# Kernel optimization log

Measured on AMD Instinct MI355X. Metric: run time of the kernel, lower is better.

## Reference

```python
import jax, jax.numpy as jnp
import numpy as np

E = 1024   # embed_dim
H = 16     # num_heads
D = E // H # head dim = 64
NUM_BUCKETS = 32
MAX_DISTANCE = 128


def _relative_position_bucket(rel, num_buckets=NUM_BUCKETS, max_distance=MAX_DISTANCE):
    # T5-style bucketing (bidirectional): sign half + log-spaced far buckets.
    nb = num_buckets // 2
    buckets = (rel > 0).astype(jnp.int32) * nb
    rel = jnp.abs(rel)
    max_exact = nb // 2
    is_small = rel < max_exact
    # clamp to >=1 before log to avoid -inf on the masked-out branch
    rel_f = jnp.maximum(rel, 1).astype(jnp.float32)
    large = max_exact + (
        jnp.log(rel_f / max_exact) / np.log(max_distance / max_exact) * (nb - max_exact)
    ).astype(jnp.int32)
    large = jnp.minimum(large, nb - 1)
    return buckets + jnp.where(is_small, rel, large)


def setup_inputs() -> dict:
    key = jax.random.key(0)
    ks = jax.random.split(key, 6)
    B, S, K = 2, 2048, 2048
    w = 0.02
    return {
        "hidden_states": jax.random.normal(ks[0], (B, S, E), jnp.float32),
        "key_value_states": jax.random.normal(ks[1], (B, K, E), jnp.float32),
        "Wq": jax.random.normal(ks[2], (E, E), jnp.float32) * w,
        "Wkv": jax.random.normal(ks[3], (E, 2 * E), jnp.float32) * w,
        "Wo": jax.random.normal(ks[4], (E, E), jnp.float32) * w,
        "rel_bias": jax.random.normal(ks[5], (NUM_BUCKETS, H), jnp.float32) * w,
    }


def reference(hidden_states, key_value_states, Wq, Wkv, Wo, rel_bias):
    B, S, _ = hidden_states.shape
    K = key_value_states.shape[1]
    # projections (no bias, no 1/sqrt(d) scaling — T5 style)
    q = (hidden_states @ Wq).reshape(B, S, H, D).transpose(0, 2, 1, 3)      # [B,H,S,D]
    kv = (key_value_states @ Wkv).reshape(B, K, 2, H, D)
    k = kv[:, :, 0].transpose(0, 2, 1, 3)                                   # [B,H,K,D]
    v = kv[:, :, 1].transpose(0, 2, 1, 3)                                   # [B,H,K,D]
    scores = jnp.einsum('bhsd,bhkd->bhsk', q, k)                            # [B,H,S,K]
    # relative position bias
    rel = jnp.arange(K)[None, :] - jnp.arange(S)[:, None]                   # [S,K]
    buckets = _relative_position_bucket(rel)                                # [S,K]
    bias = rel_bias[buckets].transpose(2, 0, 1)[None]                       # [1,H,S,K]
    scores = scores + bias
    attn = jax.nn.softmax(scores.astype(jnp.float32), axis=-1).astype(scores.dtype)
    out = jnp.einsum('bhsk,bhkd->bshd', attn, v).reshape(B, S, E)
    return out @ Wo
```

## Files before the change

kernel.cpp:

```cpp
#include <hip/hip_runtime.h>
#include <hip/hip_bf16.h>
#include <math.h>

typedef __hip_bfloat16 bf16;
typedef __bf16 bf16x4 __attribute__((ext_vector_type(4)));
typedef __bf16 bf16x8 __attribute__((ext_vector_type(8)));
typedef float f32x4 __attribute__((ext_vector_type(4)));
typedef float f32x16 __attribute__((ext_vector_type(16)));
typedef unsigned short us4 __attribute__((ext_vector_type(4)));

#define LOG2E 1.44269504088896340736f

#if defined(__has_builtin)
#if __has_builtin(__builtin_amdgcn_exp2f)
#define EXP2(x) __builtin_amdgcn_exp2f(x)
#else
#define EXP2(x) exp2f(x)
#endif
#else
#define EXP2(x) exp2f(x)
#endif


__device__ inline __bf16 f2b(float f) {
  __hip_bfloat16 h = __float2bfloat16(f);
  return *reinterpret_cast<__bf16*>(&h);
}
__device__ inline unsigned short b2u(float f) {
  __hip_bfloat16 h = __float2bfloat16(f);
  return *reinterpret_cast<unsigned short*>(&h);
}
__device__ inline unsigned short b2u_fast(float f) {
  union { float f; unsigned u; } v;
  v.f = f;
  return (unsigned short)((v.u + 0x8000u) >> 16);
}
__device__ inline bf16x8 ld16(const bf16* p) {
  bf16x4 lo = *(const bf16x4*)p;
  bf16x4 hi = *(const bf16x4*)(p + 4);
  return __builtin_shufflevector(lo, hi, 0, 1, 2, 3, 4, 5, 6, 7);
}
__device__ inline void st16(bf16* p, uint4 v) {
  *(uint2*)p = make_uint2(v.x, v.y);
  *(uint2*)(p + 4) = make_uint2(v.z, v.w);
}
__device__ inline us4 shfl32_us4(us4 v) {
  uint2 u = *(uint2*)&v;
  u.x = __shfl_xor(u.x, 32);
  u.y = __shfl_xor(u.y, 32);
  return *(us4*)&u;
}
__device__ inline bf16x8 mk8(us4 lo, us4 hi) {
  bf16x4 l = *(bf16x4*)&lo;
  bf16x4 h = *(bf16x4*)&hi;
  return __builtin_shufflevector(l, h, 0, 1, 2, 3, 4, 5, 6, 7);
}
__device__ inline void async16(const bf16* g, bf16* l) {
  __builtin_amdgcn_global_load_lds(
      (const __attribute__((address_space(1))) unsigned int*)g,
      (__attribute__((address_space(3))) unsigned int*)l, 16, 0, 0);
}

__global__ void cast2_k(const float* __restrict__ a, const float* __restrict__ b,
                        bf16* __restrict__ oa, bf16* __restrict__ ob) {
  int gid = blockIdx.x * 256 + threadIdx.x;
  const float* in = (gid < 524288) ? a : b;
  bf16* out = (gid < 524288) ? oa : ob;
  int i = (gid & 524287) * 8;
  float4 a0 = *(const float4*)(in + i);
  float4 a1 = *(const float4*)(in + i + 4);
  bf16x8 v;
  v[0] = f2b(a0.x); v[1] = f2b(a0.y); v[2] = f2b(a0.z); v[3] = f2b(a0.w);
  v[4] = f2b(a1.x); v[5] = f2b(a1.y); v[6] = f2b(a1.z); v[7] = f2b(a1.w);
  *(bf16x8*)(out + i) = v;
}

__global__ void prep_k(const float* __restrict__ Wq, const float* __restrict__ Wkv,
                       const float* __restrict__ Wo, const float* __restrict__ rel_bias,
                       bf16* __restrict__ WqT, bf16* __restrict__ WkvT,
                       bf16* __restrict__ WoT, float* __restrict__ lut) {
  __shared__ float tile[32][33];
  int z = blockIdx.z;
  int tx = threadIdx.x, ty = threadIdx.y;
  if (z == 3) {
    if (blockIdx.y != 0 || blockIdx.x >= 16) return;
    int r = blockIdx.x * 256 + ty * 32 + tx;
    int rel = r - 2048;
    int bkt = rel > 0 ? 16 : 0;
    int ar = rel < 0 ? -rel : rel;
    int idx;
    if (ar < 8) {
      idx = bkt + ar;
    } else {
      double t = log((double)ar / 8.0) / log(16.0) * 8.0;
      int lg = 8 + (int)t;
      if (lg > 15) lg = 15;
      idx = bkt + lg;
    }
    for (int h = 0; h < 16; ++h)
      lut[h * 4096 + r] = rel_bias[idx * 16 + h] * LOG2E;
    return;
  }
  const float* in = z == 0 ? Wq : (z == 1 ? Wkv : Wo);
  bf16* out = z == 0 ? WqT : (z == 1 ? WkvT : WoT);
  int cols = z == 1 ? 2048 : 1024;
  int c0 = blockIdx.x * 32;
  if (c0 >= cols) return;
  int r0 = blockIdx.y * 32;
  for (int i = ty; i < 32; i += 8)
    tile[i][tx] = in[(size_t)(r0 + i) * cols + c0 + tx];
  __syncthreads();
  for (int i = ty; i < 32; i += 8)
    out[(size_t)(c0 + i) * 1024 + r0 + tx] = __float2bfloat16(tile[tx][i]);
}

__global__ __launch_bounds__(256) void gemm_qkv_k(const bf16* __restrict__ hbf,
                                                  const bf16* __restrict__ kbf,
                                                  const bf16* __restrict__ WqT,
                                                  const bf16* __restrict__ WkvT,
                                                  bf16* __restrict__ Qb,
                                                  bf16* __restrict__ Kb,
                                                  bf16* __restrict__ Vt) {
  __shared__ __align__(16) bf16 As[128 * 32];
  __shared__ __align__(16) bf16 Bs[128 * 32];
  const int tid = threadIdx.x;
  const int lane = tid & 63;
  const int w = tid >> 6;
  const int wm = (w >> 1) * 64;
  const int wn = (w & 1) * 64;
  const int l15 = lane & 15;
  const int quad = lane >> 4;
  const int srow = lane >> 2;
  const int skg = lane & 3;

  const bool isQ = blockIdx.y < 8;
  const bf16* A = isQ ? hbf : kbf;
  const bf16* Bt = isQ ? WqT : WkvT;
  const int n0 = (isQ ? blockIdx.y : blockIdx.y - 8) * 128;
  const int m0 = blockIdx.x * 128;
  const bool isV = (!isQ) && (n0 >= 1024);

  f32x4 acc[4][4];
#pragma unroll
  for (int i = 0; i < 4; ++i)
#pragma unroll
    for (int j = 0; j < 4; ++j) acc[i][j] = (f32x4){0.f, 0.f, 0.f, 0.f};

  for (int k0 = 0; k0 < 1024; k0 += 32) {
    __syncthreads();
#pragma unroll
    for (int rep = 0; rep < 2; ++rep) {
      int seg = w * 2 + rep;
      async16(A + (size_t)(m0 + seg * 16 + srow) * 1024 + k0 + skg * 8, As + seg * 512);
      async16(Bt + (size_t)(n0 + seg * 16 + srow) * 1024 + k0 + skg * 8, Bs + seg * 512);
    }
    __syncthreads();
    bf16x8 af[4], bfr[4];
#pragma unroll
    for (int i = 0; i < 4; ++i)
      af[i] = *(const bf16x8*)(As + (wm + i * 16 + l15) * 32 + quad * 8);
#pragma unroll
    for (int j = 0; j < 4; ++j)
      bfr[j] = *(const bf16x8*)(Bs + (wn + j * 16 + l15) * 32 + quad * 8);
    if (isV) {
#pragma unroll
      for (int i = 0; i < 4; ++i)
#pragma unroll
        for (int j = 0; j < 4; ++j)
          acc[i][j] = __builtin_amdgcn_mfma_f32_16x16x32_bf16(af[i], bfr[j], acc[i][j], 0, 0, 0);
    } else {
#pragma unroll
      for (int i = 0; i < 4; ++i)
#pragma unroll
        for (int j = 0; j < 4; ++j)
          acc[i][j] = __builtin_amdgcn_mfma_f32_16x16x32_bf16(bfr[j], af[i], acc[i][j], 0, 0, 0);
    }
  }

  if (isV) {
#pragma unroll
    for (int i = 0; i < 4; ++i) {
      int gmb = m0 + wm + i * 16 + quad * 4;
      int b = gmb >> 11, kp = gmb & 2047;
#pragma unroll
      for (int j = 0; j < 4; ++j) {
        int gn = n0 + wn + j * 16 + l15;
        int h = (gn >> 6) & 15, d = gn & 63;
        us4 pk;
#pragma unroll
        for (int r = 0; r < 4; ++r) pk[r] = b2u(acc[i][j][r]);
        *(us4*)(Vt + ((((size_t)b * 16 + h) * 64 + d) << 11) + kp) = pk;
      }
    }
    return;
  }
  const float scale = isQ ? LOG2E : 1.0f;
  bf16* dst = isQ ? Qb : Kb;
#pragma unroll
  for (int i = 0; i < 4; ++i) {
    int gm = m0 + wm + i * 16 + l15;
    int b = gm >> 11, s = gm & 2047;
#pragma unroll
    for (int j = 0; j < 4; ++j) {
      int gn = n0 + wn + j * 16 + quad * 4;
      int h = (gn >> 6) & 15, d0 = gn & 63;
      us4 pk;
#pragma unroll
      for (int r = 0; r < 4; ++r) pk[r] = b2u(acc[i][j][r] * scale);
      *(us4*)(dst + ((((size_t)b * 16 + h) * 2048 + s) << 6) + d0) = pk;
    }
  }
}

__global__ __launch_bounds__(256) void gemm_o_k(const bf16* __restrict__ A,
                                                const bf16* __restrict__ Bt,
                                                float* __restrict__ C0) {
  __shared__ __align__(16) bf16 As[128 * 32];
  __shared__ __align__(16) bf16 Bs[64 * 32];
  const int tid = threadIdx.x;
  const int lane = tid & 63;
  const int w = tid >> 6;
  const int wm = w * 32;
  const int m0 = blockIdx.x * 128;
  const int n0 = blockIdx.y * 64;
  const int l15 = lane & 15;
  const int quad = lane >> 4;
  const int srow = lane >> 2;
  const int skg = lane & 3;

  f32x4 acc[2][4];
#pragma unroll
  for (int i = 0; i < 2; ++i)
#pragma unroll
    for (int j = 0; j < 4; ++j) acc[i][j] = (f32x4){0.f, 0.f, 0.f, 0.f};

  for (int k0 = 0; k0 < 1024; k0 += 32) {
    __syncthreads();
#pragma unroll
    for (int rep = 0; rep < 2; ++rep) {
      int seg = w * 2 + rep;
      async16(A + (size_t)(m0 + seg * 16 + srow) * 1024 + k0 + skg * 8, As + seg * 512);
    }
    async16(Bt + (size_t)(n0 + w * 16 + srow) * 1024 + k0 + skg * 8, Bs + w * 512);
    __syncthreads();
    bf16x8 af[2], bfr[4];
#pragma unroll
    for (int i = 0; i < 2; ++i)
      af[i] = *(const bf16x8*)(As + (wm + i * 16 + l15) * 32 + quad * 8);
#pragma unroll
    for (int j = 0; j < 4; ++j)
      bfr[j] = *(const bf16x8*)(Bs + (j * 16 + l15) * 32 + quad * 8);
#pragma unroll
    for (int i = 0; i < 2; ++i)
#pragma unroll
      for (int j = 0; j < 4; ++j)
        acc[i][j] = __builtin_amdgcn_mfma_f32_16x16x32_bf16(bfr[j], af[i], acc[i][j], 0, 0, 0);
  }
#pragma unroll
  for (int i = 0; i < 2; ++i) {
    int gm = m0 + wm + i * 16 + l15;
#pragma unroll
    for (int j = 0; j < 4; ++j) {
      int gn = n0 + j * 16 + quad * 4;
      *(f32x4*)(C0 + (size_t)gm * 1024 + gn) = acc[i][j];
    }
  }
}

#define STK 68
#define SVK 136
#define KS_OFF 8704
#define VS_OFF 43520
__global__ __launch_bounds__(512, 2) void attn_k(const bf16* __restrict__ Qb,
                                                 const bf16* __restrict__ Kb,
                                                 const bf16* __restrict__ Vt,
                                                 const float* __restrict__ lut,
                                                 bf16* __restrict__ Ob) {
  __shared__ __align__(16) char smem[78336];
  float* lbias = (float*)smem;
  bf16* Ksb = (bf16*)(smem + KS_OFF);
  bf16* Vsb = (bf16*)(smem + VS_OFF);

  const int tid = threadIdx.x;
  const int lane = tid & 63;
  const int w = tid >> 6;
  const int wq = w & 3;
  const int kg = w >> 2;
  const int t256 = tid & 255;
  const int q31 = lane & 31;
  const int half = lane >> 5;

  bf16* Ks = Ksb + kg * (128 * STK);
  bf16* Vs = Vsb + kg * (64 * SVK);

  const int wg = blockIdx.x;
  const int xcd = wg & 7;
  const int slot = wg >> 3;
  const int bh = xcd * 4 + (slot >> 4);
  const int qt = slot & 15;
  const int h = bh & 15, b = bh >> 4;
  const int qb = qt * 128;

  const int gbase = h * 4096 + 1921 - qb;
  for (int t = tid; t < 2175; t += 512) lbias[t] = lut[gbase + t];

  const size_t base = (size_t)bh * 2048 * 64;
  const size_t vbase = (size_t)bh * 64 * 2048;
  const int qg = qb + wq * 32 + q31;

  bf16x8 qf[4];
#pragma unroll
  for (int c = 0; c < 4; ++c)
    qf[c] = *(const bf16x8*)(Qb + base + (size_t)qg * 64 + c * 16 + half * 8);

  f32x16 oacc[2];
#pragma unroll
  for (int dj = 0; dj < 2; ++dj)
#pragma unroll
    for (int r = 0; r < 16; ++r) oacc[dj][r] = 0.f;
  float l_run = 0.f;

  const int kt0 = kg * 128;

  for (int it = 0; it < 8; ++it) {
    const int kt = it * 256 + kt0;
    __syncthreads();
    {
      uint4 kr[4], vr[4];
#pragma unroll
      for (int rep = 0; rep < 4; ++rep) {
        int slot2 = t256 + rep * 256;
        kr[rep] = *(const uint4*)(Kb + base + (size_t)(kt + (slot2 >> 3)) * 64 + (slot2 & 7) * 8);
        vr[rep] = *(const uint4*)(Vt + vbase + (size_t)(slot2 >> 4) * 2048 + kt + (slot2 & 15) * 8);
      }
#pragma unroll
      for (int rep = 0; rep < 4; ++rep) {
        int slot2 = t256 + rep * 256;
        st16(Ks + (slot2 >> 3) * STK + (slot2 & 7) * 8, kr[rep]);
        st16(Vs + (slot2 >> 4) * SVK + (slot2 & 15) * 8, vr[rep]);
      }
    }
    __syncthreads();

    const int xbase = kt + 127 + 4 * half - wq * 32 - q31;
#pragma unroll
    for (int mt = 0; mt < 4; ++mt) {
      f32x16 sacc;
#pragma unroll
      for (int a2 = 0; a2 < 4; ++a2)
#pragma unroll
        for (int rr = 0; rr < 4; ++rr)
          sacc[4 * a2 + rr] = lbias[xbase + mt * 32 + 8 * a2 + rr];
#pragma unroll
      for (int c = 0; c < 4; ++c) {
        bf16x8 kf = ld16(Ks + (mt * 32 + q31) * STK + c * 16 + half * 8);
        sacc = __builtin_amdgcn_mfma_f32_32x32x16_bf16(kf, qf[c], sacc, 0, 0, 0);
      }

      us4 ownq[4];
      f32x4 sv = (f32x4){0.f, 0.f, 0.f, 0.f};
#pragma unroll
      for (int a = 0; a < 4; ++a) {
        us4 pk;
#pragma unroll
        for (int rr = 0; rr < 4; ++rr) {
          float p = EXP2(sacc[4 * a + rr]);
          sv[rr] += p;
          pk[rr] = b2u_fast(p);
        }
        ownq[a] = pk;
      }
      l_run += (sv[0] + sv[1]) + (sv[2] + sv[3]);

      us4 rcv0 = shfl32_us4(half ? ownq[0] : ownq[1]);
      us4 rcv1 = shfl32_us4(half ? ownq[2] : ownq[3]);

#pragma unroll
      for (int p = 0; p < 2; ++p) {
        us4 rc = p ? rcv1 : rcv0;
        bf16x8 pfc = half ? mk8(rc, ownq[2 * p + 1]) : mk8(ownq[2 * p], rc);
#pragma unroll
        for (int dj = 0; dj < 2; ++dj) {
          bf16x8 vf = ld16(Vs + (dj * 32 + q31) * SVK + (mt * 2 + p) * 16 + half * 8);
          oacc[dj] = __builtin_amdgcn_mfma_f32_32x32x16_bf16(vf, pfc, oacc[dj], 0, 0, 0);
        }
      }
    }
  }

  l_run += __shfl_xor(l_run, 32);

  __syncthreads();
  float* mbuf = (float*)smem;
  if (kg) {
    float* p = mbuf + ((size_t)(wq * 64 + lane)) * 35;
    p[0] = l_run;
#pragma unroll
    for (int dj = 0; dj < 2; ++dj)
#pragma unroll
      for (int r = 0; r < 16; ++r) p[1 + dj * 16 + r] = oacc[dj][r];
  }
  __syncthreads();
  if (kg) return;

  const float* p = mbuf + ((size_t)(wq * 64 + lane)) * 35;
  float inv = 1.0f / (l_run + p[0]);

#pragma unroll
  for (int dj = 0; dj < 2; ++dj)
#pragma unroll
    for (int g = 0; g < 4; ++g) {
      us4 pk;
#pragma unroll
      for (int rr = 0; rr < 4; ++rr)
        pk[rr] = b2u((oacc[dj][4 * g + rr] + p[1 + dj * 16 + 4 * g + rr]) * inv);
      int d0 = dj * 32 + 8 * g + 4 * half;
      *(us4*)(Ob + ((size_t)(b * 2048 + qg)) * 1024 + h * 64 + d0) = pk;
    }
}

extern "C" void kernel_launch(void* const* d_in, const int* in_sizes, int n_in,
                              void* d_out, int out_size, void* d_ws, size_t ws_size,
                              hipStream_t stream) {
  const float* hidden = (const float*)d_in[0];
  const float* kvs    = (const float*)d_in[1];
  const float* Wq     = (const float*)d_in[2];
  const float* Wkv    = (const float*)d_in[3];
  const float* Wo     = (const float*)d_in[4];
  const float* relb   = (const float*)d_in[5];
  float* out = (float*)d_out;

  char* ws = (char*)d_ws;
  bf16* WqT  = (bf16*)(ws + (size_t)0);
  bf16* WkvT = (bf16*)(ws + ((size_t)2 << 20));
  bf16* WoT  = (bf16*)(ws + ((size_t)6 << 20));
  bf16* Ob   = (bf16*)(ws + ((size_t)8 << 20));
  bf16* hbf  = Ob;
  bf16* Qb   = (bf16*)(ws + ((size_t)16 << 20));
  bf16* Kb   = (bf16*)(ws + ((size_t)24 << 20));
  bf16* Vt   = (bf16*)(ws + ((size_t)32 << 20));
  float* LUT = (float*)(ws + ((size_t)40 << 20));
  bf16* kbf  = (bf16*)d_out;

  prep_k<<<dim3(64, 32, 4), dim3(32, 8), 0, stream>>>(Wq, Wkv, Wo, relb, WqT, WkvT, WoT, LUT);
  cast2_k<<<4096, 256, 0, stream>>>(hidden, kvs, hbf, kbf);
  gemm_qkv_k<<<dim3(32, 24), 256, 0, stream>>>(hbf, kbf, WqT, WkvT, Qb, Kb, Vt);
  attn_k<<<dim3(512), 512, 0, stream>>>(Qb, Kb, Vt, LUT, Ob);
  gemm_o_k<<<dim3(32, 16), 256, 0, stream>>>(Ob, WoT, out);
}
```

Baseline: 218.8 us.

## Merge input cast into prep kernel and swizzle GEMM blocks per XCD

The fp32-to-bf16 cast of the activations becomes extra z-slices of the prep kernel, which removes one kernel launch. The QKV and output-projection GEMMs switch to a 1D grid whose block index is remapped. Blocks that land on the same XCD (round-robin by block id mod 8) then share the same weight column tile, which should improve L2 reuse on MI355X's per-XCD caches. The remap assumes exactly 8 XCDs and fixed grid sizes.

```diff
diff --git a/kernel.cpp b/kernel.cpp
--- a/kernel.cpp
+++ b/kernel.cpp
@@ -61,27 +61,29 @@
       (__attribute__((address_space(3))) unsigned int*)l, 16, 0, 0);
 }
 
-__global__ void cast2_k(const float* __restrict__ a, const float* __restrict__ b,
-                        bf16* __restrict__ oa, bf16* __restrict__ ob) {
-  int gid = blockIdx.x * 256 + threadIdx.x;
-  const float* in = (gid < 524288) ? a : b;
-  bf16* out = (gid < 524288) ? oa : ob;
-  int i = (gid & 524287) * 8;
-  float4 a0 = *(const float4*)(in + i);
-  float4 a1 = *(const float4*)(in + i + 4);
-  bf16x8 v;
-  v[0] = f2b(a0.x); v[1] = f2b(a0.y); v[2] = f2b(a0.z); v[3] = f2b(a0.w);
-  v[4] = f2b(a1.x); v[5] = f2b(a1.y); v[6] = f2b(a1.z); v[7] = f2b(a1.w);
-  *(bf16x8*)(out + i) = v;
-}
-
 __global__ void prep_k(const float* __restrict__ Wq, const float* __restrict__ Wkv,
                        const float* __restrict__ Wo, const float* __restrict__ rel_bias,
+                       const float* __restrict__ hidden, const float* __restrict__ kvs,
                        bf16* __restrict__ WqT, bf16* __restrict__ WkvT,
-                       bf16* __restrict__ WoT, float* __restrict__ lut) {
+                       bf16* __restrict__ WoT, float* __restrict__ lut,
+                       bf16* __restrict__ hbf, bf16* __restrict__ kbf) {
   __shared__ float tile[32][33];
   int z = blockIdx.z;
   int tx = threadIdx.x, ty = threadIdx.y;
+  if (z >= 4) {
+    int bidFlat = (z - 4) * 2048 + blockIdx.y * 64 + blockIdx.x;
+    int gid = bidFlat * 256 + ty * 32 + tx;
+    const float* in = (gid < 524288) ? hidden : kvs;
+    bf16* out = (gid < 524288) ? hbf : kbf;
+    int i = (gid & 524287) * 8;
+    float4 a0 = *(const float4*)(in + i);
+    float4 a1 = *(const float4*)(in + i + 4);
+    bf16x8 v;
+    v[0] = f2b(a0.x); v[1] = f2b(a0.y); v[2] = f2b(a0.z); v[3] = f2b(a0.w);
+    v[4] = f2b(a1.x); v[5] = f2b(a1.y); v[6] = f2b(a1.z); v[7] = f2b(a1.w);
+    *(bf16x8*)(out + i) = v;
+    return;
+  }
   if (z == 3) {
     if (blockIdx.y != 0 || blockIdx.x >= 16) return;
     int r = blockIdx.x * 256 + ty * 32 + tx;
@@ -133,11 +135,17 @@
   const int srow = lane >> 2;
   const int skg = lane & 3;
 
-  const bool isQ = blockIdx.y < 8;
+  const int wg = blockIdx.x;
+  const int xcd = wg & 7;
+  const int slot = wg >> 3;
+  const int by = xcd * 3 + (slot >> 5);
+  const int bx = slot & 31;
+
+  const bool isQ = by < 8;
   const bf16* A = isQ ? hbf : kbf;
   const bf16* Bt = isQ ? WqT : WkvT;
-  const int n0 = (isQ ? blockIdx.y : blockIdx.y - 8) * 128;
-  const int m0 = blockIdx.x * 128;
+  const int n0 = (isQ ? by : by - 8) * 128;
+  const int m0 = bx * 128;
   const bool isV = (!isQ) && (n0 >= 1024);
 
   f32x4 acc[4][4];
@@ -221,8 +229,15 @@
   const int lane = tid & 63;
   const int w = tid >> 6;
   const int wm = w * 32;
-  const int m0 = blockIdx.x * 128;
-  const int n0 = blockIdx.y * 64;
+
+  const int wg = blockIdx.x;
+  const int xcd = wg & 7;
+  const int slot = wg >> 3;
+  const int by = xcd * 2 + (slot >> 5);
+  const int bx = slot & 31;
+  const int m0 = bx * 128;
+  const int n0 = by * 64;
+
   const int l15 = lane & 15;
   const int quad = lane >> 4;
   const int srow = lane >> 2;
@@ -442,9 +457,9 @@
   float* LUT = (float*)(ws + ((size_t)40 << 20));
   bf16* kbf  = (bf16*)d_out;
 
-  prep_k<<<dim3(64, 32, 4), dim3(32, 8), 0, stream>>>(Wq, Wkv, Wo, relb, WqT, WkvT, WoT, LUT);
-  cast2_k<<<4096, 256, 0, stream>>>(hidden, kvs, hbf, kbf);
-  gemm_qkv_k<<<dim3(32, 24), 256, 0, stream>>>(hbf, kbf, WqT, WkvT, Qb, Kb, Vt);
+  prep_k<<<dim3(64, 32, 6), dim3(32, 8), 0, stream>>>(Wq, Wkv, Wo, relb, hidden, kvs,
+                                                      WqT, WkvT, WoT, LUT, hbf, kbf);
+  gemm_qkv_k<<<dim3(768), 256, 0, stream>>>(hbf, kbf, WqT, WkvT, Qb, Kb, Vt);
   attn_k<<<dim3(512), 512, 0, stream>>>(Qb, Kb, Vt, LUT, Ob);
-  gemm_o_k<<<dim3(32, 16), 256, 0, stream>>>(Ob, WoT, out);
-}
+  gemm_o_k<<<dim3(512), 256, 0, stream>>>(Ob, WoT, out);
+}
```

Result: no change. 219.2 us (+0.2%).
